# Performance work log

Hardware: AMD Instinct MI355X
Metric: run time of the kernel (lower is better)

Reference implementation:

```python
import jax, jax.numpy as jnp
import numpy as np

# Sampled-neighborhood cascade sizes (src->dst per layer) and edge counts
N0, N1, N2, N3 = 400000, 200000, 100000, 50000
E1, E2, E3 = 500000, 300000, 150000
DIN, DH = 128, 128


def setup_inputs() -> dict:
    key = jax.random.key(0)
    ks = jax.random.split(key, 24)
    inp = {}
    inp['x'] = jax.random.normal(ks[0], (N0, DIN), jnp.float32)
    inp['src1'] = jax.random.randint(ks[1], (E1,), 0, N0, dtype=jnp.int64)
    inp['dst1'] = jax.random.randint(ks[2], (E1,), 0, N1, dtype=jnp.int64)
    inp['src2'] = jax.random.randint(ks[3], (E2,), 0, N1, dtype=jnp.int64)
    inp['dst2'] = jax.random.randint(ks[4], (E2,), 0, N2, dtype=jnp.int64)
    inp['src3'] = jax.random.randint(ks[5], (E3,), 0, N2, dtype=jnp.int64)
    inp['dst3'] = jax.random.randint(ks[6], (E3,), 0, N3, dtype=jnp.int64)
    # SAGEConv params: lin_l (on aggregated neighbors, with bias), lin_r (root, no bias)
    dims = [(DIN, DH), (DH, DH), (DH, DH)]
    for i, (di, do) in enumerate(dims, start=1):
        s = 1.0 / np.sqrt(di)
        inp[f'Wl{i}'] = jax.random.uniform(ks[6 + 4 * i - 3], (di, do), jnp.float32, -s, s)
        inp[f'Wr{i}'] = jax.random.uniform(ks[6 + 4 * i - 2], (di, do), jnp.float32, -s, s)
        inp[f'b{i}'] = jax.random.uniform(ks[6 + 4 * i - 1], (do,), jnp.float32, -s, s)
        inp[f'a{i}'] = jnp.full((do,), 0.25, jnp.float32)  # PReLU per-channel init
    return inp


def _sage_prelu(x_src, n_dst, src, dst, Wl, Wr, b, alpha):
    # mean aggregation over incoming edges (PyG SAGEConv default aggr='mean')
    x_dst = x_src[:n_dst]                                   # [n_dst, d]
    msg = x_src[src]                                        # [E, d] gather
    summed = jax.ops.segment_sum(msg, dst, num_segments=n_dst)
    cnt = jax.ops.segment_sum(jnp.ones(src.shape[0], x_src.dtype), dst,
                              num_segments=n_dst)
    mean = summed / jnp.maximum(cnt, 1.0)[:, None]
    out = mean @ Wl + b + x_dst @ Wr                        # lin_l(aggr) + lin_r(root)
    return jnp.where(out > 0, out, alpha * out)             # per-channel PReLU


def reference(x, src1, dst1, src2, dst2, src3, dst3,
              Wl1, Wr1, b1, a1, Wl2, Wr2, b2, a2, Wl3, Wr3, b3, a3):
    h = _sage_prelu(x, N1, src1, dst1, Wl1, Wr1, b1, a1)
    h = _sage_prelu(h, N2, src2, dst2, Wl2, Wr2, b2, a2)
    h = _sage_prelu(h, N3, src3, dst3, Wl3, Wr3, b3, a3)
    return h  # [N3, DH]
```

## Files before the change

### kernel.cpp

```cpp
#include <hip/hip_runtime.h>


constexpr int cN0 = 400000, cN1 = 200000, cN2 = 100000, cN3 = 50000;
constexpr int cE1 = 500000, cE2 = 300000, cE3 = 150000;
constexpr int cNT = cN1 + cN2 + cN3;
constexpr int cET = cE1 + cE2 + cE3;

#define NDIV_UP(a, b) (((a) + (b) - 1) / (b))

typedef __attribute__((ext_vector_type(8))) short bf16x8;
typedef __attribute__((ext_vector_type(4))) float f32x4;
typedef __attribute__((ext_vector_type(4))) unsigned u32x4;

__device__ __forceinline__ unsigned fbits(float f) {
  return __builtin_bit_cast(unsigned, f);
}
__device__ __forceinline__ float ffrom(unsigned u) {
  return __builtin_bit_cast(float, u);
}
__device__ __forceinline__ unsigned short f2bf(float f) {
  unsigned u = fbits(f);
  unsigned r = u + 0x7FFFu + ((u >> 16) & 1u);
  return (unsigned short)(r >> 16);
}

__global__ void detect_idx64_kernel(const long long* __restrict__ p, int E,
                                    long long nmax, int* __restrict__ flag) {
  int t = threadIdx.x;
  int n = E < 512 ? E : 512;
  int bad = 0;
  for (int i = t; i < n; i += 64) {
    long long v = p[i];
    if (v < 0 || v >= nmax) bad = 1;
  }
  unsigned long long b = __ballot(bad);
  if (t == 0) *flag = (b == 0ull) ? 1 : 0;
}

__device__ __forceinline__ int load_idx(const void* p, int i, int flag) {
  return flag ? (int)((const long long*)p)[i] : ((const int*)p)[i];
}

__global__ void hist3_kernel(const void* __restrict__ d1, const void* __restrict__ d2,
                             const void* __restrict__ d3, const int* __restrict__ flag,
                             int* __restrict__ CNT) {
  int e = blockIdx.x * 256 + threadIdx.x;
  if (e >= cET) return;
  int f = *flag;
  int d;
  if (e < cE1) d = load_idx(d1, e, f);
  else if (e < cE1 + cE2) d = cN1 + load_idx(d2, e - cE1, f);
  else d = cN1 + cN2 + load_idx(d3, e - cE1 - cE2, f);
  atomicAdd(&CNT[d], 1);
}

__global__ __launch_bounds__(256) void scan_reduce(const int* __restrict__ cnt,
                                                   int n, int* __restrict__ bsum) {
  __shared__ int s[256];
  int t = threadIdx.x;
  int base = blockIdx.x * 1024 + t * 4;
  int v = 0;
  if (base + 3 < n) {
    int4 c = *(const int4*)(cnt + base);
    v = c.x + c.y + c.z + c.w;
  } else {
    for (int i = 0; i < 4; ++i)
      if (base + i < n) v += cnt[base + i];
  }
  s[t] = v;
  __syncthreads();
  for (int off = 128; off > 0; off >>= 1) {
    if (t < off) s[t] += s[t + off];
    __syncthreads();
  }
  if (t == 0) bsum[blockIdx.x] = s[0];
}

__global__ __launch_bounds__(256) void scan_bsums(int* __restrict__ bsum, int nb) {
  __shared__ int s[256];
  int t = threadIdx.x;
  int v0 = (2 * t < nb) ? bsum[2 * t] : 0;
  int v1 = (2 * t + 1 < nb) ? bsum[2 * t + 1] : 0;
  int p = v0 + v1;
  s[t] = p;
  __syncthreads();
  for (int off = 1; off < 256; off <<= 1) {
    int x = (t >= off) ? s[t - off] : 0;
    __syncthreads();
    s[t] += x;
    __syncthreads();
  }
  int excl = s[t] - p;
  if (2 * t < nb) bsum[2 * t] = excl;
  if (2 * t + 1 < nb) bsum[2 * t + 1] = excl + v0;
}

__global__ __launch_bounds__(256) void scan_final(const int* __restrict__ cnt,
                                                  int n, const int* __restrict__ bsum,
                                                  int* __restrict__ offs) {
  __shared__ int s[256];
  int t = threadIdx.x;
  int base = blockIdx.x * 1024 + t * 4;
  int v0 = 0, v1 = 0, v2 = 0, v3 = 0;
  if (base + 3 < n) {
    int4 c = *(const int4*)(cnt + base);
    v0 = c.x; v1 = c.y; v2 = c.z; v3 = c.w;
  } else {
    if (base + 0 < n) v0 = cnt[base + 0];
    if (base + 1 < n) v1 = cnt[base + 1];
    if (base + 2 < n) v2 = cnt[base + 2];
  }
  int tsum = v0 + v1 + v2 + v3;
  s[t] = tsum;
  __syncthreads();
  for (int off = 1; off < 256; off <<= 1) {
    int x = (t >= off) ? s[t - off] : 0;
    __syncthreads();
    s[t] += x;
    __syncthreads();
  }
  int excl = s[t] - tsum;
  int o = bsum[blockIdx.x] + excl;
  if (base + 0 < n) offs[base + 0] = o;
  o += v0;
  if (base + 1 < n) offs[base + 1] = o;
  o += v1;
  if (base + 2 < n) offs[base + 2] = o;
  o += v2;
  if (base + 3 < n) offs[base + 3] = o;
}

__global__ void fill3_kernel(const void* __restrict__ s1, const void* __restrict__ d1,
                             const void* __restrict__ s2, const void* __restrict__ d2,
                             const void* __restrict__ s3, const void* __restrict__ d3,
                             const int* __restrict__ flag,
                             int* __restrict__ OFFS, int* __restrict__ EID) {
  int e = blockIdx.x * 256 + threadIdx.x;
  if (e >= cET) return;
  int f = *flag;
  int s, d;
  if (e < cE1) {
    s = load_idx(s1, e, f);
    d = load_idx(d1, e, f);
  } else if (e < cE1 + cE2) {
    int i = e - cE1;
    s = load_idx(s2, i, f);
    d = cN1 + load_idx(d2, i, f);
  } else {
    int i = e - cE1 - cE2;
    s = load_idx(s3, i, f);
    d = cN1 + cN2 + load_idx(d3, i, f);
  }
  int pos = atomicAdd(&OFFS[d], 1);
  EID[pos] = s;
}

__global__ void pack_w3_kernel(const float* __restrict__ Wl1, const float* __restrict__ Wr1,
                               const float* __restrict__ Wl2, const float* __restrict__ Wr2,
                               const float* __restrict__ Wl3, const float* __restrict__ Wr3,
                               unsigned short* __restrict__ wpk) {
  int idx = blockIdx.x * 256 + threadIdx.x;
  if (idx >= 3 * 16384) return;
  int L = idx >> 14;
  int r = idx & 16383;
  const float* Wl = L == 0 ? Wl1 : (L == 1 ? Wl2 : Wl3);
  const float* Wr = L == 0 ? Wr1 : (L == 1 ? Wr2 : Wr3);
  unsigned short* o = wpk + L * 32768;
  int j = r & 7, l = (r >> 3) & 63, cf = (r >> 9) & 7, ks = r >> 12;
  int k = ks * 32 + (l >> 4) * 8 + j;
  int col = cf * 16 + (l & 15);
  o[r] = f2bf(Wl[k * 128 + col]);
  o[16384 + r] = f2bf(Wr[k * 128 + col]);
}

template <bool SRCF32>
__global__ __launch_bounds__(256) void gather_kernel(
    const void* __restrict__ hsrc, const int* __restrict__ OFFS,
    const int* __restrict__ EID, int rowoff,
    unsigned short* __restrict__ meanB, int n) {
  const int wid = blockIdx.x * 4 + (threadIdx.x >> 6);
  const int lane = threadIdx.x & 63;
  const int r0 = wid * 4;
  if (r0 >= n) return;
  const int gr0 = rowoff + r0;

  int b[5];
  b[0] = (gr0 == 0) ? 0 : OFFS[gr0 - 1];
#pragma unroll
  for (int j = 0; j < 4; ++j)
    b[j + 1] = (r0 + j < n) ? OFFS[gr0 + j] : -1;
#pragma unroll
  for (int j = 0; j < 4; ++j)
    if (b[j + 1] < 0) b[j + 1] = b[j];

  float a0[4] = {0.f, 0.f, 0.f, 0.f};
  float a1[4] = {0.f, 0.f, 0.f, 0.f};

  const int bend = b[4];
  if (bend > b[0]) {
    const int blast = bend - 1;
    for (int e = b[0]; e < bend; e += 8) {
      int sid[8];
#pragma unroll
      for (int k = 0; k < 8; ++k) {
        const int ei = e + k;
        sid[k] = EID[ei <= blast ? ei : blast];
      }
      float v0[8], v1[8];
#pragma unroll
      for (int k = 0; k < 8; ++k) {
        if (SRCF32) {
          const float2 v = *(const float2*)((const float*)hsrc +
                                            (size_t)sid[k] * 128 + lane * 2);
          v0[k] = v.x;
          v1[k] = v.y;
        } else {
          const unsigned u = *(const unsigned*)((const unsigned short*)hsrc +
                                                (size_t)sid[k] * 128 + lane * 2);
          v0[k] = ffrom(u << 16);
          v1[k] = ffrom(u & 0xFFFF0000u);
        }
      }
#pragma unroll
      for (int k = 0; k < 8; ++k) {
        const int ei = e + k;
#pragma unroll
        for (int j = 0; j < 4; ++j) {
          const bool p = (ei >= b[j]) & (ei < b[j + 1]);
          a0[j] += p ? v0[k] : 0.f;
          a1[j] += p ? v1[k] : 0.f;
        }
      }
    }
  }

#pragma unroll
  for (int j = 0; j < 4; ++j) {
    const int row = r0 + j;
    if (row < n) {
      const int cnt = b[j + 1] - b[j];
      const float inv = (cnt > 0) ? 1.0f / (float)cnt : 0.0f;
      const unsigned o = (unsigned)f2bf(a0[j] * inv) |
                         ((unsigned)f2bf(a1[j] * inv) << 16);
      *(unsigned*)(meanB + (size_t)row * 128 + lane * 2) = o;
    }
  }
}

template <bool XF32, bool OUTF32>
__global__ __launch_bounds__(256, 2) void gemm_kernel(
    const unsigned short* __restrict__ meanB, const void* __restrict__ xsrc,
    const unsigned short* __restrict__ W,
    const float* __restrict__ bias, const float* __restrict__ alpha,
    void* __restrict__ outp, int n) {
  __shared__ __align__(16) unsigned short wlds[32768];
  const int tid = threadIdx.x;
  const int lane = tid & 63;
  const int wv = tid >> 6;
  const int rbase = blockIdx.x * 128 + wv * 32;
  const int g = lane >> 4;
  const int r16 = lane & 15;

  bf16x8 am[2][4], ax[2][4];
  float4 xr[2][4][2];
#pragma unroll
  for (int t = 0; t < 2; ++t) {
    const int row = rbase + t * 16 + r16;
    const bool ok = row < n;
#pragma unroll
    for (int ks = 0; ks < 4; ++ks) {
      if (ok) {
        am[t][ks] = *(const bf16x8*)(meanB + (size_t)row * 128 + ks * 32 + g * 8);
        if (XF32) {
          const float* xp = (const float*)xsrc + (size_t)row * 128 + ks * 32 + g * 8;
          xr[t][ks][0] = *(const float4*)(xp);
          xr[t][ks][1] = *(const float4*)(xp + 4);
        } else {
          ax[t][ks] = *(const bf16x8*)((const unsigned short*)xsrc +
                                       (size_t)row * 128 + ks * 32 + g * 8);
        }
      } else {
        am[t][ks] = (bf16x8)0;
        if (XF32) {
          xr[t][ks][0] = make_float4(0.f, 0.f, 0.f, 0.f);
          xr[t][ks][1] = make_float4(0.f, 0.f, 0.f, 0.f);
        } else {
          ax[t][ks] = (bf16x8)0;
        }
      }
    }
  }

  {
    const float4* Wg = (const float4*)W;
    float4* Ws = (float4*)wlds;
#pragma unroll
    for (int i = 0; i < 16; ++i)
      Ws[i * 256 + tid] = Wg[i * 256 + tid];
  }
  __syncthreads();

  if (XF32) {
#pragma unroll
    for (int t = 0; t < 2; ++t)
#pragma unroll
      for (int ks = 0; ks < 4; ++ks) {
        const float* xv = (const float*)&xr[t][ks][0];
        u32x4 w;
#pragma unroll
        for (int p = 0; p < 4; ++p)
          w[p] = (unsigned)f2bf(xv[2 * p]) | ((unsigned)f2bf(xv[2 * p + 1]) << 16);
        ax[t][ks] = __builtin_bit_cast(bf16x8, w);
      }
  }

  f32x4 acc[2][8] = {};
#pragma unroll
  for (int ks = 0; ks < 4; ++ks) {
    const unsigned short* wb = wlds + ks * 4096 + lane * 8;
#pragma unroll
    for (int cf = 0; cf < 8; ++cf) {
      const unsigned short* wp = wb + cf * 512;
      bf16x8 wl = *(const bf16x8*)(wp);
      bf16x8 wr = *(const bf16x8*)(wp + 16384);
#pragma unroll
      for (int t = 0; t < 2; ++t) {
        acc[t][cf] = __builtin_amdgcn_mfma_f32_16x16x32_bf16(am[t][ks], wl, acc[t][cf], 0, 0, 0);
        acc[t][cf] = __builtin_amdgcn_mfma_f32_16x16x32_bf16(ax[t][ks], wr, acc[t][cf], 0, 0, 0);
      }
    }
  }

  const int ocol0 = lane & 15;
  const int orow_off = (lane >> 4) * 4;
#pragma unroll
  for (int cf = 0; cf < 8; ++cf) {
    const int ocol = cf * 16 + ocol0;
    const float b = bias[ocol];
    const float a = alpha[ocol];
#pragma unroll
    for (int t = 0; t < 2; ++t) {
      const int orb = rbase + t * 16 + orow_off;
#pragma unroll
      for (int i = 0; i < 4; ++i) {
        const int orow = orb + i;
        if (orow < n) {
          float v = acc[t][cf][i] + b;
          v = v > 0.f ? v : a * v;
          if (OUTF32) {
            ((float*)outp)[(size_t)orow * 128 + ocol] = v;
          } else {
            ((unsigned short*)outp)[(size_t)orow * 128 + ocol] = f2bf(v);
          }
        }
      }
    }
  }
}

extern "C" void kernel_launch(void* const* d_in, const int* in_sizes, int n_in,
                              void* d_out, int out_size, void* d_ws, size_t ws_size,
                              hipStream_t stream) {
  const float* x = (const float*)d_in[0];
  const void* src1 = d_in[1];
  const void* dst1 = d_in[2];
  const void* src2 = d_in[3];
  const void* dst2 = d_in[4];
  const void* src3 = d_in[5];
  const void* dst3 = d_in[6];
  const float* Wl1 = (const float*)d_in[7];
  const float* Wr1 = (const float*)d_in[8];
  const float* b1  = (const float*)d_in[9];
  const float* a1  = (const float*)d_in[10];
  const float* Wl2 = (const float*)d_in[11];
  const float* Wr2 = (const float*)d_in[12];
  const float* b2  = (const float*)d_in[13];
  const float* a2  = (const float*)d_in[14];
  const float* Wl3 = (const float*)d_in[15];
  const float* Wr3 = (const float*)d_in[16];
  const float* b3  = (const float*)d_in[17];
  const float* a3  = (const float*)d_in[18];

  unsigned short* M1 = (unsigned short*)d_ws;
  unsigned short* M2 = M1 + (size_t)cN1 * 128;
  unsigned short* M3 = M2 + (size_t)cN2 * 128;
  int* CNT = (int*)(M3 + (size_t)cN3 * 128);
  int* OFFS = CNT + cNT;
  int* EID = OFFS + cNT;
  int* bsum = EID + cET;
  int* flag = bsum + 1024;
  unsigned short* wpk = (unsigned short*)(flag + 64);

  const int nb = NDIV_UP(cNT, 1024);

  detect_idx64_kernel<<<1, 64, 0, stream>>>((const long long*)src1, cE1,
                                            (long long)cN0, flag);
  pack_w3_kernel<<<192, 256, 0, stream>>>(Wl1, Wr1, Wl2, Wr2, Wl3, Wr3, wpk);
  hipMemsetAsync(CNT, 0, (size_t)cNT * sizeof(int), stream);
  hist3_kernel<<<NDIV_UP(cET, 256), 256, 0, stream>>>(dst1, dst2, dst3, flag, CNT);
  scan_reduce<<<nb, 256, 0, stream>>>(CNT, cNT, bsum);
  scan_bsums<<<1, 256, 0, stream>>>(bsum, nb);
  scan_final<<<nb, 256, 0, stream>>>(CNT, cNT, bsum, OFFS);
  fill3_kernel<<<NDIV_UP(cET, 256), 256, 0, stream>>>(src1, dst1, src2, dst2,
                                                      src3, dst3, flag, OFFS, EID);

  gather_kernel<true><<<NDIV_UP(cN1, 16), 256, 0, stream>>>(
      x, OFFS, EID, 0, M1, cN1);
  gemm_kernel<true, false><<<NDIV_UP(cN1, 128), 256, 0, stream>>>(
      M1, x, wpk, b1, a1, M1, cN1);

  gather_kernel<false><<<NDIV_UP(cN2, 16), 256, 0, stream>>>(
      M1, OFFS, EID, cN1, M2, cN2);
  gemm_kernel<false, false><<<NDIV_UP(cN2, 128), 256, 0, stream>>>(
      M2, M1, wpk + 32768, b2, a2, M2, cN2);

  gather_kernel<false><<<NDIV_UP(cN3, 16), 256, 0, stream>>>(
      M2, OFFS, EID, cN1 + cN2, M3, cN3);
  gemm_kernel<false, true><<<NDIV_UP(cN3, 128), 256, 0, stream>>>(
      M3, M2, wpk + 65536, b3, a3, d_out, cN3);
}
```

Before: 346.5 us.

## Pre-convert input features to bf16 and fuse conversion with histogram and weight packing

Adds a fused kernel that converts x from fp32 to a bf16 copy while also building the destination histogram and packing weights, replacing two separate launches. The layer-1 gather and GEMM then read bf16 rows instead of fp32, halving their per-row bytes. This adds a full streaming pass over x plus a bf16 write, and reuses the M2/M3 workspace region for the bf16 copy.

```diff
diff --git a/kernel.cpp b/kernel.cpp
--- a/kernel.cpp
+++ b/kernel.cpp
@@ -41,17 +41,54 @@
   return flag ? (int)((const long long*)p)[i] : ((const int*)p)[i];
 }
 
-__global__ void hist3_kernel(const void* __restrict__ d1, const void* __restrict__ d2,
-                             const void* __restrict__ d3, const int* __restrict__ flag,
-                             int* __restrict__ CNT) {
-  int e = blockIdx.x * 256 + threadIdx.x;
-  if (e >= cET) return;
-  int f = *flag;
-  int d;
-  if (e < cE1) d = load_idx(d1, e, f);
-  else if (e < cE1 + cE2) d = cN1 + load_idx(d2, e - cE1, f);
-  else d = cN1 + cN2 + load_idx(d3, e - cE1 - cE2, f);
-  atomicAdd(&CNT[d], 1);
+constexpr int NCONV = (cN0 * 128) / 2048;
+constexpr int NHIST = NDIV_UP(cET, 256);
+constexpr int NPACK = NDIV_UP(3 * 16384, 256);
+
+__global__ __launch_bounds__(256) void convhistpack_kernel(
+    const float* __restrict__ x, unsigned short* __restrict__ xb,
+    const void* __restrict__ d1, const void* __restrict__ d2,
+    const void* __restrict__ d3, const int* __restrict__ flag,
+    int* __restrict__ CNT,
+    const float* __restrict__ Wl1, const float* __restrict__ Wr1,
+    const float* __restrict__ Wl2, const float* __restrict__ Wr2,
+    const float* __restrict__ Wl3, const float* __restrict__ Wr3,
+    unsigned short* __restrict__ wpk) {
+  const int bid = blockIdx.x;
+  const int tid = threadIdx.x;
+  if (bid < NCONV) {
+    const size_t base = (size_t)bid * 2048 + tid * 8;
+    const float4 v0 = *(const float4*)(x + base);
+    const float4 v1 = *(const float4*)(x + base + 4);
+    u32x4 o;
+    o[0] = (unsigned)f2bf(v0.x) | ((unsigned)f2bf(v0.y) << 16);
+    o[1] = (unsigned)f2bf(v0.z) | ((unsigned)f2bf(v0.w) << 16);
+    o[2] = (unsigned)f2bf(v1.x) | ((unsigned)f2bf(v1.y) << 16);
+    o[3] = (unsigned)f2bf(v1.z) | ((unsigned)f2bf(v1.w) << 16);
+    *(u32x4*)(xb + base) = o;
+  } else if (bid < NCONV + NHIST) {
+    const int e = (bid - NCONV) * 256 + tid;
+    if (e >= cET) return;
+    const int f = *flag;
+    int d;
+    if (e < cE1) d = load_idx(d1, e, f);
+    else if (e < cE1 + cE2) d = cN1 + load_idx(d2, e - cE1, f);
+    else d = cN1 + cN2 + load_idx(d3, e - cE1 - cE2, f);
+    atomicAdd(&CNT[d], 1);
+  } else {
+    const int idx = (bid - NCONV - NHIST) * 256 + tid;
+    if (idx >= 3 * 16384) return;
+    const int L = idx >> 14;
+    const int r = idx & 16383;
+    const float* Wl = L == 0 ? Wl1 : (L == 1 ? Wl2 : Wl3);
+    const float* Wr = L == 0 ? Wr1 : (L == 1 ? Wr2 : Wr3);
+    unsigned short* o = wpk + L * 32768;
+    const int j = r & 7, l = (r >> 3) & 63, cf = (r >> 9) & 7, ks = r >> 12;
+    const int k = ks * 32 + (l >> 4) * 8 + j;
+    const int col = cf * 16 + (l & 15);
+    o[r] = f2bf(Wl[k * 128 + col]);
+    o[16384 + r] = f2bf(Wr[k * 128 + col]);
+  }
 }
 
 __global__ __launch_bounds__(256) void scan_reduce(const int* __restrict__ cnt,
@@ -155,27 +192,8 @@
   EID[pos] = s;
 }
 
-__global__ void pack_w3_kernel(const float* __restrict__ Wl1, const float* __restrict__ Wr1,
-                               const float* __restrict__ Wl2, const float* __restrict__ Wr2,
-                               const float* __restrict__ Wl3, const float* __restrict__ Wr3,
-                               unsigned short* __restrict__ wpk) {
-  int idx = blockIdx.x * 256 + threadIdx.x;
-  if (idx >= 3 * 16384) return;
-  int L = idx >> 14;
-  int r = idx & 16383;
-  const float* Wl = L == 0 ? Wl1 : (L == 1 ? Wl2 : Wl3);
-  const float* Wr = L == 0 ? Wr1 : (L == 1 ? Wr2 : Wr3);
-  unsigned short* o = wpk + L * 32768;
-  int j = r & 7, l = (r >> 3) & 63, cf = (r >> 9) & 7, ks = r >> 12;
-  int k = ks * 32 + (l >> 4) * 8 + j;
-  int col = cf * 16 + (l & 15);
-  o[r] = f2bf(Wl[k * 128 + col]);
-  o[16384 + r] = f2bf(Wr[k * 128 + col]);
-}
-
-template <bool SRCF32>
 __global__ __launch_bounds__(256) void gather_kernel(
-    const void* __restrict__ hsrc, const int* __restrict__ OFFS,
+    const unsigned short* __restrict__ hsrc, const int* __restrict__ OFFS,
     const int* __restrict__ EID, int rowoff,
     unsigned short* __restrict__ meanB, int n) {
   const int wid = blockIdx.x * 4 + (threadIdx.x >> 6);
@@ -209,17 +227,9 @@
       float v0[8], v1[8];
 #pragma unroll
       for (int k = 0; k < 8; ++k) {
-        if (SRCF32) {
-          const float2 v = *(const float2*)((const float*)hsrc +
-                                            (size_t)sid[k] * 128 + lane * 2);
-          v0[k] = v.x;
-          v1[k] = v.y;
-        } else {
-          const unsigned u = *(const unsigned*)((const unsigned short*)hsrc +
-                                                (size_t)sid[k] * 128 + lane * 2);
-          v0[k] = ffrom(u << 16);
-          v1[k] = ffrom(u & 0xFFFF0000u);
-        }
+        const unsigned u = *(const unsigned*)(hsrc + (size_t)sid[k] * 128 + lane * 2);
+        v0[k] = ffrom(u << 16);
+        v1[k] = ffrom(u & 0xFFFF0000u);
       }
 #pragma unroll
       for (int k = 0; k < 8; ++k) {
@@ -247,9 +257,10 @@
   }
 }
 
-template <bool XF32, bool OUTF32>
+template <bool OUTF32>
 __global__ __launch_bounds__(256, 2) void gemm_kernel(
-    const unsigned short* __restrict__ meanB, const void* __restrict__ xsrc,
+    const unsigned short* __restrict__ meanB,
+    const unsigned short* __restrict__ xsrc,
     const unsigned short* __restrict__ W,
     const float* __restrict__ bias, const float* __restrict__ alpha,
     void* __restrict__ outp, int n) {
@@ -262,7 +273,6 @@
   const int r16 = lane & 15;
 
   bf16x8 am[2][4], ax[2][4];
-  float4 xr[2][4][2];
 #pragma unroll
   for (int t = 0; t < 2; ++t) {
     const int row = rbase + t * 16 + r16;
@@ -271,22 +281,10 @@
     for (int ks = 0; ks < 4; ++ks) {
       if (ok) {
         am[t][ks] = *(const bf16x8*)(meanB + (size_t)row * 128 + ks * 32 + g * 8);
-        if (XF32) {
-          const float* xp = (const float*)xsrc + (size_t)row * 128 + ks * 32 + g * 8;
-          xr[t][ks][0] = *(const float4*)(xp);
-          xr[t][ks][1] = *(const float4*)(xp + 4);
-        } else {
-          ax[t][ks] = *(const bf16x8*)((const unsigned short*)xsrc +
-                                       (size_t)row * 128 + ks * 32 + g * 8);
-        }
+        ax[t][ks] = *(const bf16x8*)(xsrc + (size_t)row * 128 + ks * 32 + g * 8);
       } else {
         am[t][ks] = (bf16x8)0;
-        if (XF32) {
-          xr[t][ks][0] = make_float4(0.f, 0.f, 0.f, 0.f);
-          xr[t][ks][1] = make_float4(0.f, 0.f, 0.f, 0.f);
-        } else {
-          ax[t][ks] = (bf16x8)0;
-        }
+        ax[t][ks] = (bf16x8)0;
       }
     }
   }
@@ -299,20 +297,6 @@
       Ws[i * 256 + tid] = Wg[i * 256 + tid];
   }
   __syncthreads();
-
-  if (XF32) {
-#pragma unroll
-    for (int t = 0; t < 2; ++t)
-#pragma unroll
-      for (int ks = 0; ks < 4; ++ks) {
-        const float* xv = (const float*)&xr[t][ks][0];
-        u32x4 w;
-#pragma unroll
-        for (int p = 0; p < 4; ++p)
-          w[p] = (unsigned)f2bf(xv[2 * p]) | ((unsigned)f2bf(xv[2 * p + 1]) << 16);
-        ax[t][ks] = __builtin_bit_cast(bf16x8, w);
-      }
-  }
 
   f32x4 acc[2][8] = {};
 #pragma unroll
@@ -382,9 +366,10 @@
   const float* a3  = (const float*)d_in[18];
 
   unsigned short* M1 = (unsigned short*)d_ws;
-  unsigned short* M2 = M1 + (size_t)cN1 * 128;
-  unsigned short* M3 = M2 + (size_t)cN2 * 128;
-  int* CNT = (int*)(M3 + (size_t)cN3 * 128);
+  unsigned short* xb = M1 + (size_t)cN1 * 128;
+  unsigned short* M2 = xb;
+  unsigned short* M3 = xb + (size_t)cN2 * 128;
+  int* CNT = (int*)(xb + (size_t)cN0 * 128);
   int* OFFS = CNT + cNT;
   int* EID = OFFS + cNT;
   int* bsum = EID + cET;
@@ -395,27 +380,28 @@
 
   detect_idx64_kernel<<<1, 64, 0, stream>>>((const long long*)src1, cE1,
                                             (long long)cN0, flag);
-  pack_w3_kernel<<<192, 256, 0, stream>>>(Wl1, Wr1, Wl2, Wr2, Wl3, Wr3, wpk);
   hipMemsetAsync(CNT, 0, (size_t)cNT * sizeof(int), stream);
-  hist3_kernel<<<NDIV_UP(cET, 256), 256, 0, stream>>>(dst1, dst2, dst3, flag, CNT);
+  convhistpack_kernel<<<NCONV + NHIST + NPACK, 256, 0, stream>>>(
+      x, xb, dst1, dst2, dst3, flag, CNT,
+      Wl1, Wr1, Wl2, Wr2, Wl3, Wr3, wpk);
   scan_reduce<<<nb, 256, 0, stream>>>(CNT, cNT, bsum);
   scan_bsums<<<1, 256, 0, stream>>>(bsum, nb);
   scan_final<<<nb, 256, 0, stream>>>(CNT, cNT, bsum, OFFS);
   fill3_kernel<<<NDIV_UP(cET, 256), 256, 0, stream>>>(src1, dst1, src2, dst2,
                                                       src3, dst3, flag, OFFS, EID);
 
-  gather_kernel<true><<<NDIV_UP(cN1, 16), 256, 0, stream>>>(
-      x, OFFS, EID, 0, M1, cN1);
-  gemm_kernel<true, false><<<NDIV_UP(cN1, 128), 256, 0, stream>>>(
-      M1, x, wpk, b1, a1, M1, cN1);
-
-  gather_kernel<false><<<NDIV_UP(cN2, 16), 256, 0, stream>>>(
+  gather_kernel<<<NDIV_UP(cN1, 16), 256, 0, stream>>>(
+      xb, OFFS, EID, 0, M1, cN1);
+  gemm_kernel<false><<<NDIV_UP(cN1, 128), 256, 0, stream>>>(
+      M1, xb, wpk, b1, a1, M1, cN1);
+
+  gather_kernel<<<NDIV_UP(cN2, 16), 256, 0, stream>>>(
       M1, OFFS, EID, cN1, M2, cN2);
-  gemm_kernel<false, false><<<NDIV_UP(cN2, 128), 256, 0, stream>>>(
+  gemm_kernel<false><<<NDIV_UP(cN2, 128), 256, 0, stream>>>(
       M2, M1, wpk + 32768, b2, a2, M2, cN2);
 
-  gather_kernel<false><<<NDIV_UP(cN3, 16), 256, 0, stream>>>(
+  gather_kernel<<<NDIV_UP(cN3, 16), 256, 0, stream>>>(
       M2, OFFS, EID, cN1 + cN2, M3, cN3);
-  gemm_kernel<false, true><<<NDIV_UP(cN3, 128), 256, 0, stream>>>(
+  gemm_kernel<true><<<NDIV_UP(cN3, 128), 256, 0, stream>>>(
       M3, M2, wpk + 65536, b3, a3, d_out, cN3);
 }
```

New measurement: 364.8 us. 1.05x slower.
